# Performance work log

Hardware: AMD Instinct MI355X
Metric: run time of the kernel (lower is better)

The kernel has to match this reference:

```python
import jax, jax.numpy as jnp
import numpy as np

N_NODES = 100000
N_EDGES = 1600000
NFEAT, NHID, NCLASS = 512, 256, 40
ALPHA = 1.0
N_POWERS = 10


def setup_inputs() -> dict:
    key = jax.random.key(0)
    ks = jax.random.split(key, 8)
    x = jax.random.normal(ks[0], (N_NODES, NFEAT), dtype=jnp.float32)
    edge_index = jax.random.randint(ks[1], (2, N_EDGES), 0, N_NODES)
    # Kaiming-ish init, scale = 1/sqrt(fan_in)
    W1 = jax.random.normal(ks[2], (NHID, NFEAT), dtype=jnp.float32) / np.sqrt(NFEAT)
    b1 = jnp.zeros((NHID,), jnp.float32)
    W2 = jax.random.normal(ks[3], (NHID, NHID), dtype=jnp.float32) / np.sqrt(NHID)
    b2 = jnp.zeros((NHID,), jnp.float32)
    W3 = jax.random.normal(ks[4], (NCLASS, NHID), dtype=jnp.float32) / np.sqrt(NHID)
    b3 = jnp.zeros((NCLASS,), jnp.float32)
    return {"x": x, "edge_index": edge_index, "W1": W1, "b1": b1,
            "W2": W2, "b2": b2, "W3": W3, "b3": b3}


def reference(x, edge_index, W1, b1, W2, b2, W3, b3):
    N = x.shape[0]
    # --- build DA-normalized adjacency with self-loops (to_normalized_sparsetensor, mode='DA') ---
    self_loop = jnp.arange(N)
    rows = jnp.concatenate([edge_index[0], self_loop])  # [E+N]
    cols = jnp.concatenate([edge_index[1], self_loop])  # [E+N]
    deg = jax.ops.segment_sum(jnp.ones(rows.shape[0], x.dtype), rows, num_segments=N)
    # DA mode: rows scaled by deg_inv_sqrt^2 == deg^{-1}
    deg_inv = jnp.where(deg > 0, 1.0 / deg, 0.0)
    w = deg_inv[rows]  # per-edge weight, [E+N]

    def spmm(v):  # A @ v, v: [N, C]
        return jax.ops.segment_sum(w[:, None] * v[cols], rows, num_segments=N)

    # --- MLP (dropout=0, eval mode) ---
    h = jax.nn.relu(x @ W1.T + b1)
    h = jax.nn.relu(h @ W2.T + b2)
    h = h @ W3.T + b3  # [N, NCLASS]

    # --- approximate_invphi_x power iteration (beta=0 branch) ---
    c1 = ALPHA / (1.0 + ALPHA)
    c2 = 1.0 / (1.0 + ALPHA)
    invphi = h
    for _ in range(N_POWERS):
        invphi = c1 * spmm(invphi) + c2 * h
    return invphi
```

## Files before the change

### kernel.cpp

```cpp
#include <hip/hip_runtime.h>
#include <type_traits>

#define N_NODES 100000
#define N_EDGES 1600000
#define NFEAT 512
#define NHID 256
#define NCLASS 40
#define NPAD 100096
#define NPAD2 100352

#define NBUCK 196
#define BROWS 512
#define NBLK_BIN 256
#define EPB 6250

#define CDUM 1916000
#define COLN 1916032

#define ZA (N_NODES * 32)
#define ZB (N_NODES * 8)
#define BLK_A 3125
#define BLK_B 391

typedef __bf16 bf16;
typedef __bf16 bf16x8 __attribute__((ext_vector_type(8)));
typedef __bf16 bf16x4 __attribute__((ext_vector_type(4)));
typedef float f32x4 __attribute__((ext_vector_type(4)));
typedef int i32x4 __attribute__((ext_vector_type(4)));


__global__ __launch_bounds__(256) void bin_count(const int* __restrict__ rows,
                                                 int* __restrict__ bcnt) {
    __shared__ int hist[NBUCK];
    int t = threadIdx.x, b = blockIdx.x;
    for (int i = t; i < NBUCK; i += 256) hist[i] = 0;
    __syncthreads();
    int base = b * EPB;
    for (int i = t; i < EPB; i += 256) atomicAdd(&hist[rows[base + i] >> 9], 1);
    __syncthreads();
    for (int i = t; i < NBUCK; i += 256) bcnt[i * NBLK_BIN + b] = hist[i];
}

__global__ __launch_bounds__(256) void bin_scan(const int* __restrict__ bcnt,
                                                int* __restrict__ boff2,
                                                int* __restrict__ btot) {
    __shared__ int sh[256];
    int t = threadIdx.x, bu = blockIdx.x;
    int v = bcnt[bu * 256 + t];
    sh[t] = v;
    __syncthreads();
    for (int off = 1; off < 256; off <<= 1) {
        int x = (t >= off) ? sh[t - off] : 0;
        __syncthreads();
        sh[t] += x;
        __syncthreads();
    }
    boff2[t * NBUCK + bu] = sh[t] - v;
    if (t == 255) btot[bu] = sh[255];
}

__global__ __launch_bounds__(256) void base_scan(const int* __restrict__ btot,
                                                 int* __restrict__ bbase) {
    __shared__ int sh[256];
    int t = threadIdx.x;
    int v = (t < NBUCK) ? btot[t] : 0;
    sh[t] = v;
    __syncthreads();
    for (int off = 1; off < 256; off <<= 1) {
        int x = (t >= off) ? sh[t - off] : 0;
        __syncthreads();
        sh[t] += x;
        __syncthreads();
    }
    if (t < NBUCK) bbase[t] = sh[t] - v;
    if (t == NBUCK - 1) bbase[NBUCK] = sh[t];
}

__global__ __launch_bounds__(256) void bin_scatter(const int* __restrict__ rows,
                                                   const int* __restrict__ cols,
                                                   const int* __restrict__ boff2,
                                                   const int* __restrict__ bbase,
                                                   int* __restrict__ binned) {
    __shared__ int cur[NBUCK];
    int t = threadIdx.x, b = blockIdx.x;
    for (int i = t; i < NBUCK; i += 256) cur[i] = bbase[i] + boff2[b * NBUCK + i];
    __syncthreads();
    int base = b * EPB;
    for (int i = t; i < EPB; i += 256) {
        int r = rows[base + i], c = cols[base + i];
        int pos = atomicAdd(&cur[r >> 9], 1);
        binned[pos] = ((r & 511) << 17) | c;
    }
}

__global__ __launch_bounds__(256) void bucket_csr(const int* __restrict__ binned,
                                                  const int* __restrict__ bbase,
                                                  int2* __restrict__ rowptr2,
                                                  int* __restrict__ colidx,
                                                  float* __restrict__ dinv) {
    __shared__ int cnt[BROWS];
    __shared__ int pref[BROWS];
    __shared__ int psum[256];
    int t = threadIdx.x, bu = blockIdx.x;
    cnt[t] = 0;
    cnt[t + 256] = 0;
    __syncthreads();
    int base = bbase[bu], end = bbase[bu + 1];
    for (int i = base + t; i < end; i += 256) atomicAdd(&cnt[binned[i] >> 17], 1);
    __syncthreads();
    int c0 = cnt[2 * t], c1 = cnt[2 * t + 1];
    int p0 = (c0 + 3) & ~3, p1 = (c1 + 3) & ~3;
    psum[t] = p0 + p1;
    __syncthreads();
    for (int off = 1; off < 256; off <<= 1) {
        int x = (t >= off) ? psum[t - off] : 0;
        __syncthreads();
        psum[t] += x;
        __syncthreads();
    }
    int pex = psum[t] - (p0 + p1);
    pref[2 * t] = pex;
    pref[2 * t + 1] = pex + p0;
    __syncthreads();
    int pbase = (base & ~3) + bu * 1600;
#pragma unroll
    for (int j = 0; j < 2; j++) {
        int idx = t + j * 256;
        int grow = bu * BROWS + idx;
        int rc = cnt[idx];
        int st = pbase + pref[idx];
        int en = st + ((rc + 3) & ~3);
        if (grow < N_NODES) {
            rowptr2[grow] = make_int2(st, en);
            dinv[grow] = 0.5f / (float)(rc + 1);
            for (int k = st + rc; k < en; k++) colidx[k] = N_NODES;
        } else {
            rowptr2[grow] = make_int2(0, 0);
        }
        pref[idx] = st;
    }
    __syncthreads();
    for (int i = base + t; i < end; i += 256) {
        int v = binned[i];
        int pos = atomicAdd(&pref[v >> 17], 1);
        colidx[pos] = v & 0x1FFFF;
    }
}


__global__ void cvt_f2b(const float* __restrict__ a, bf16* __restrict__ b, int n) {
    int i = blockIdx.x * 256 + threadIdx.x;
    if (i < n) b[i] = (bf16)a[i];
}

__global__ void pad_w3(const float* __restrict__ W3, const float* __restrict__ b3,
                       bf16* __restrict__ W3p, float* __restrict__ b3p) {
    int i = blockIdx.x * 256 + threadIdx.x;
    int r = i >> 8;
    W3p[i] = (bf16)((r < NCLASS) ? W3[(size_t)r * 256 + (i & 255)] : 0.f);
    if (i < 64) b3p[i] = (i < NCLASS) ? b3[i] : 0.f;
}

__global__ void zero_dummy(bf16* vAi, bf16* vA0, bf16* vA1,
                           bf16* vBi, bf16* vB0, bf16* vB1,
                           int* colidx) {
    int i = threadIdx.x;
    if (i < 32) {
        vAi[(size_t)ZA + i] = (bf16)0.f;
        vA0[(size_t)ZA + i] = (bf16)0.f;
        vA1[(size_t)ZA + i] = (bf16)0.f;
    }
    if (i < 8) {
        vBi[(size_t)ZB + i] = (bf16)0.f;
        vB0[(size_t)ZB + i] = (bf16)0.f;
        vB1[(size_t)ZB + i] = (bf16)0.f;
        colidx[CDUM + i] = N_NODES;
    }
}


template <int BN, typename AT, bool RELU, int OUTMODE>
__global__ __launch_bounds__(256) void gemm_mfma(const AT* __restrict__ A,
                                                 const bf16* __restrict__ B,
                                                 const float* __restrict__ bias,
                                                 bf16* __restrict__ Cb,
                                                 float* __restrict__ hA,
                                                 float* __restrict__ hB,
                                                 bf16* __restrict__ vA0,
                                                 bf16* __restrict__ vB0,
                                                 int M, int K, int Nout) {
    constexpr int LDT = 40;
    constexpr int WTM = (BN == 128) ? 64 : 32;
    constexpr int MI = WTM / 16;
    constexpr int WMC = 128 / WTM;
    constexpr int BG = BN / 64;
    constexpr bool AF32 = std::is_same<AT, float>::value;
    __shared__ bf16 As[2][128 * LDT];
    __shared__ bf16 Bs[2][BN * LDT];

    int tid = threadIdx.x;
    int wave = tid >> 6, lane = tid & 63;
    int waveM = wave % WMC, waveN = wave / WMC;
    int lc = lane & 15, lq = lane >> 4;

    f32x4 acc[MI][4];
#pragma unroll
    for (int i = 0; i < MI; i++)
#pragma unroll
        for (int j = 0; j < 4; j++) acc[i][j] = (f32x4){0.f, 0.f, 0.f, 0.f};

    int sr = tid >> 2;
    int sc = (tid & 3) * 8;

    float4 pa[2][2];
    bf16x8 ba[2];
    bf16x8 bb[BG];

    auto LOAD = [&](int k0) {
#pragma unroll
        for (int g = 0; g < 2; g++) {
            int grow = blockIdx.y * 128 + sr + g * 64;
            if constexpr (AF32) {
                if (grow < M) {
                    const float* ap = A + (size_t)grow * K + k0 + sc;
                    pa[g][0] = *(const float4*)ap;
                    pa[g][1] = *(const float4*)(ap + 4);
                } else {
                    pa[g][0] = (float4){0.f, 0.f, 0.f, 0.f};
                    pa[g][1] = (float4){0.f, 0.f, 0.f, 0.f};
                }
            } else {
                ba[g] = (grow < M) ? *(const bf16x8*)(A + (size_t)grow * K + k0 + sc)
                                   : (bf16x8){};
            }
        }
#pragma unroll
        for (int g = 0; g < BG; g++) {
            int brow = blockIdx.x * BN + sr + g * 64;
            bb[g] = *(const bf16x8*)(B + (size_t)brow * K + k0 + sc);
        }
    };
    auto STORE = [&](int buf) {
#pragma unroll
        for (int g = 0; g < 2; g++) {
            bf16x8 val;
            if constexpr (AF32) {
                val[0] = (bf16)pa[g][0].x; val[1] = (bf16)pa[g][0].y;
                val[2] = (bf16)pa[g][0].z; val[3] = (bf16)pa[g][0].w;
                val[4] = (bf16)pa[g][1].x; val[5] = (bf16)pa[g][1].y;
                val[6] = (bf16)pa[g][1].z; val[7] = (bf16)pa[g][1].w;
            } else {
                val = ba[g];
            }
            *(bf16x8*)&As[buf][(sr + g * 64) * LDT + sc] = val;
        }
#pragma unroll
        for (int g = 0; g < BG; g++)
            *(bf16x8*)&Bs[buf][(sr + g * 64) * LDT + sc] = bb[g];
    };

    int nt = K / 32;
    LOAD(0);
    STORE(0);
    __syncthreads();
    int cur = 0;
    for (int t = 0; t < nt; t++) {
        if (t + 1 < nt) LOAD((t + 1) * 32);
        bf16x8 af[MI], bfr[4];
#pragma unroll
        for (int i = 0; i < MI; i++)
            af[i] = *(const bf16x8*)&As[cur][(waveM * WTM + i * 16 + lc) * LDT + lq * 8];
#pragma unroll
        for (int j = 0; j < 4; j++)
            bfr[j] = *(const bf16x8*)&Bs[cur][(waveN * 64 + j * 16 + lc) * LDT + lq * 8];
#pragma unroll
        for (int i = 0; i < MI; i++)
#pragma unroll
            for (int j = 0; j < 4; j++)
                acc[i][j] = __builtin_amdgcn_mfma_f32_16x16x32_bf16(af[i], bfr[j], acc[i][j], 0, 0, 0);
        if (t + 1 < nt) STORE(cur ^ 1);
        __syncthreads();
        cur ^= 1;
    }

#pragma unroll
    for (int i = 0; i < MI; i++) {
        int row0 = blockIdx.y * 128 + waveM * WTM + i * 16 + lq * 4;
#pragma unroll
        for (int j = 0; j < 4; j++) {
            int colL = waveN * 64 + j * 16 + lc;
            int col = blockIdx.x * BN + colL;
            float bv = bias[col];
#pragma unroll
            for (int reg = 0; reg < 4; reg++) {
                int rr = row0 + reg;
                if (rr < M) {
                    float v = acc[i][j][reg] + bv;
                    if (RELU) v = v > 0.f ? v : 0.f;
                    if (OUTMODE == 0) {
                        Cb[(size_t)rr * Nout + col] = (bf16)v;
                    } else {
                        if (col < 32) {
                            hA[(size_t)rr * 32 + col] = 0.5f * v;
                            vA0[(size_t)rr * 32 + col] = (bf16)v;
                        } else if (col < NCLASS) {
                            hB[(size_t)rr * 8 + (col - 32)] = 0.5f * v;
                            vB0[(size_t)rr * 8 + (col - 32)] = (bf16)v;
                        }
                    }
                }
            }
        }
    }
}


__global__ __launch_bounds__(256) void spmm_split(const bf16* __restrict__ vA,
                                                  const bf16* __restrict__ vB,
                                                  const float* __restrict__ hA,
                                                  const float* __restrict__ hB,
                                                  const int2* __restrict__ rowptr2,
                                                  const int* __restrict__ colidx,
                                                  const float* __restrict__ dinv,
                                                  bf16* __restrict__ oA,
                                                  bf16* __restrict__ oB,
                                                  float* __restrict__ outF,
                                                  int final_it) {
    int b = blockIdx.x;
    int lane = threadIdx.x & 63;
    const int* cdum = colidx + CDUM;
    if (b < BLK_A) {
        int w = b * 4 + (threadIdx.x >> 6);
        int sub = lane & 7;
        int r = w * 8 + (lane >> 3);
        int2 se = rowptr2[r];
        int sx = se.x, d = se.y - se.x;
        int m = d;
        int x = __shfl_xor(m, 8);  m = m > x ? m : x;
        x = __shfl_xor(m, 16);     m = m > x ? m : x;
        x = __shfl_xor(m, 32);     m = m > x ? m : x;
        float4 hv = *(const float4*)(hA + (size_t)r * 32 + sub * 4);
        float dv = dinv[r];
        bf16x4 sv = *(const bf16x4*)(vA + (size_t)r * 32 + sub * 4);
        float a0 = (float)sv[0], a1 = (float)sv[1], a2 = (float)sv[2], a3 = (float)sv[3];
        i32x4 cc = *(const i32x4*)(d > 0 ? colidx + sx : cdum);
        for (int i = 0; i < m; i += 4) {
            const int* np = (i + 4 < d) ? (colidx + sx + i + 4) : cdum;
            i32x4 cn = *(const i32x4*)np;
            bf16x4 g0 = *(const bf16x4*)(vA + (size_t)cc[0] * 32 + sub * 4);
            bf16x4 g1 = *(const bf16x4*)(vA + (size_t)cc[1] * 32 + sub * 4);
            bf16x4 g2 = *(const bf16x4*)(vA + (size_t)cc[2] * 32 + sub * 4);
            bf16x4 g3 = *(const bf16x4*)(vA + (size_t)cc[3] * 32 + sub * 4);
            a0 += ((float)g0[0] + (float)g1[0]) + ((float)g2[0] + (float)g3[0]);
            a1 += ((float)g0[1] + (float)g1[1]) + ((float)g2[1] + (float)g3[1]);
            a2 += ((float)g0[2] + (float)g1[2]) + ((float)g2[2] + (float)g3[2]);
            a3 += ((float)g0[3] + (float)g1[3]) + ((float)g2[3] + (float)g3[3]);
            cc = cn;
        }
        float r0 = dv * a0 + hv.x;
        float r1 = dv * a1 + hv.y;
        float r2 = dv * a2 + hv.z;
        float r3 = dv * a3 + hv.w;
        if (final_it) {
            *(float4*)(outF + (size_t)r * NCLASS + sub * 4) = (float4){r0, r1, r2, r3};
        } else {
            bf16x4 o;
            o[0] = (bf16)r0; o[1] = (bf16)r1; o[2] = (bf16)r2; o[3] = (bf16)r3;
            *(bf16x4*)(oA + (size_t)r * 32 + sub * 4) = o;
        }
    } else {
        int w = (b - BLK_A) * 4 + (threadIdx.x >> 6);
        int r = w * 64 + lane;
        int rh = (r < N_NODES) ? r : N_NODES;
        int rz = (r < N_NODES) ? r : 0;
        int2 se = rowptr2[r];
        int sx = se.x, d = se.y - se.x;
        int m = d;
#pragma unroll
        for (int off = 1; off < 64; off <<= 1) {
            int x = __shfl_xor(m, off);
            m = m > x ? m : x;
        }
        float4 h0 = *(const float4*)(hB + (size_t)rz * 8);
        float4 h1 = *(const float4*)(hB + (size_t)rz * 8 + 4);
        float dv = dinv[rz];
        bf16x8 sv = *(const bf16x8*)(vB + (size_t)rh * 8);
        float a[8];
#pragma unroll
        for (int k = 0; k < 8; k++) a[k] = (float)sv[k];
        i32x4 cc = *(const i32x4*)(d > 0 ? colidx + sx : cdum);
        for (int i = 0; i < m; i += 4) {
            const int* np = (i + 4 < d) ? (colidx + sx + i + 4) : cdum;
            i32x4 cn = *(const i32x4*)np;
            bf16x8 g0 = *(const bf16x8*)(vB + (size_t)cc[0] * 8);
            bf16x8 g1 = *(const bf16x8*)(vB + (size_t)cc[1] * 8);
            bf16x8 g2 = *(const bf16x8*)(vB + (size_t)cc[2] * 8);
            bf16x8 g3 = *(const bf16x8*)(vB + (size_t)cc[3] * 8);
#pragma unroll
            for (int k = 0; k < 8; k++)
                a[k] += ((float)g0[k] + (float)g1[k]) + ((float)g2[k] + (float)g3[k]);
            cc = cn;
        }
        if (r < N_NODES) {
            float res[8];
            res[0] = dv * a[0] + h0.x; res[1] = dv * a[1] + h0.y;
            res[2] = dv * a[2] + h0.z; res[3] = dv * a[3] + h0.w;
            res[4] = dv * a[4] + h1.x; res[5] = dv * a[5] + h1.y;
            res[6] = dv * a[6] + h1.z; res[7] = dv * a[7] + h1.w;
            if (final_it) {
                *(float4*)(outF + (size_t)r * NCLASS + 32) = (float4){res[0], res[1], res[2], res[3]};
                *(float4*)(outF + (size_t)r * NCLASS + 36) = (float4){res[4], res[5], res[6], res[7]};
            } else {
                bf16x8 o;
#pragma unroll
                for (int k = 0; k < 8; k++) o[k] = (bf16)res[k];
                *(bf16x8*)(oB + (size_t)r * 8) = o;
            }
        }
    }
}


extern "C" void kernel_launch(void* const* d_in, const int* in_sizes, int n_in,
                              void* d_out, int out_size, void* d_ws, size_t ws_size,
                              hipStream_t stream) {
    const float* x  = (const float*)d_in[0];
    const int*   ei = (const int*)d_in[1];
    const float* W1 = (const float*)d_in[2];
    const float* b1 = (const float*)d_in[3];
    const float* W2 = (const float*)d_in[4];
    const float* b2 = (const float*)d_in[5];
    const float* W3 = (const float*)d_in[6];
    const float* b3 = (const float*)d_in[7];
    float* out = (float*)d_out;
    const int* rows = ei;
    const int* cols = ei + N_EDGES;

    char* p = (char*)d_ws;
    bf16* hid1 = (bf16*)p;                 p += (size_t)N_NODES * NHID * 2;
    bf16* hid2 = (bf16*)p;                 p += (size_t)N_NODES * NHID * 2;
    float* hA  = (float*)p;                p += (size_t)N_NODES * 32 * 4;
    float* hB  = (float*)p;                p += (size_t)N_NODES * 8 * 4;
    bf16* vAi  = (bf16*)p;                 p += (size_t)(N_NODES + 1) * 32 * 2;
    bf16* vA0  = (bf16*)p;                 p += (size_t)(N_NODES + 1) * 32 * 2;
    bf16* vA1  = (bf16*)p;                 p += (size_t)(N_NODES + 1) * 32 * 2;
    bf16* vBi  = (bf16*)p;                 p += (size_t)(N_NODES + 1) * 8 * 2;
    bf16* vB0  = (bf16*)p;                 p += (size_t)(N_NODES + 1) * 8 * 2;
    bf16* vB1  = (bf16*)p;                 p += (size_t)(N_NODES + 1) * 8 * 2;
    bf16* W1b  = (bf16*)p;                 p += (size_t)NHID * NFEAT * 2;
    bf16* W2b  = (bf16*)p;                 p += (size_t)NHID * NHID * 2;
    bf16* W3p  = (bf16*)p;                 p += (size_t)64 * NHID * 2;
    float* b3p = (float*)p;                p += 64 * 4;
    int* bcnt    = (int*)p;                p += (size_t)NPAD * 4;
    int2* rowptr2 = (int2*)p;              p += (size_t)NPAD2 * 8;
    int* boff2   = (int*)p;                p += (size_t)N_NODES * 4;
    int* colidx  = (int*)p;                p += (size_t)COLN * 4;
    int* bsum    = (int*)p;                p += 512 * 4;
    float* dinv  = (float*)p;              p += (size_t)N_NODES * 4;

    int* btot  = bsum;
    int* bbase = bsum + 256;
    int* binned = (int*)hid1;

    bin_count<<<NBLK_BIN, 256, 0, stream>>>(rows, bcnt);
    bin_scan<<<NBUCK, 256, 0, stream>>>(bcnt, boff2, btot);
    base_scan<<<1, 256, 0, stream>>>(btot, bbase);
    bin_scatter<<<NBLK_BIN, 256, 0, stream>>>(rows, cols, boff2, bbase, binned);
    bucket_csr<<<NBUCK, 256, 0, stream>>>(binned, bbase, rowptr2, colidx, dinv);

    cvt_f2b<<<(NHID * NFEAT + 255) / 256, 256, 0, stream>>>(W1, W1b, NHID * NFEAT);
    cvt_f2b<<<(NHID * NHID + 255) / 256, 256, 0, stream>>>(W2, W2b, NHID * NHID);
    pad_w3<<<(64 * NHID) / 256, 256, 0, stream>>>(W3, b3, W3p, b3p);

    {
        int M = N_NODES;
        int gy = (M + 127) / 128;
        gemm_mfma<128, float, true, 0><<<dim3(2, gy), 256, 0, stream>>>(
            x, W1b, b1, hid1, nullptr, nullptr, nullptr, nullptr, M, NFEAT, NHID);
        gemm_mfma<128, bf16, true, 0><<<dim3(2, gy), 256, 0, stream>>>(
            hid1, W2b, b2, hid2, nullptr, nullptr, nullptr, nullptr, M, NHID, NHID);
        gemm_mfma<64, bf16, false, 1><<<dim3(1, gy), 256, 0, stream>>>(
            hid2, W3p, b3p, nullptr, hA, hB, vAi, vBi, M, NHID, 64);
    }

    zero_dummy<<<1, 64, 0, stream>>>(vAi, vA0, vA1, vBi, vB0, vB1, colidx);

    const bf16* sA = vAi;
    const bf16* sB = vBi;
    for (int it = 0; it < 10; it++) {
        int fin = (it == 9);
        bf16* dA = (it & 1) ? vA1 : vA0;
        bf16* dB = (it & 1) ? vB1 : vB0;
        spmm_split<<<BLK_A + BLK_B, 256, 0, stream>>>(
            sA, sB, hA, hB, rowptr2, colidx, dinv, dA, dB, out, fin);
        sA = dA;
        sB = dB;
    }
}
```

Baseline: 849.9 us.

## Deepen GEMM prefetch and widen SpMM gathers with two-stage pipelining

The GEMM main loop is unrolled by two and uses ping-pong register sets, so global loads are issued two K-tiles ahead of the MFMA work. The SpMM part A now uses 4 lanes per row with 16-byte bf16x8 gathers instead of 8 lanes with 8-byte gathers, which halves the block count. Both SpMM paths are software-pipelined to keep two groups of 4 neighbor gathers in flight. The costs are higher register pressure, extra padded iterations that read dummy indices, and an early return for out-of-range rows in part A.

```diff
diff --git a/kernel.cpp b/kernel.cpp
--- a/kernel.cpp
+++ b/kernel.cpp
@@ -19,7 +19,7 @@
 
 #define ZA (N_NODES * 32)
 #define ZB (N_NODES * 8)
-#define BLK_A 3125
+#define BLK_A 1563
 #define BLK_B 391
 
 typedef __bf16 bf16;
@@ -212,11 +212,11 @@
     int sr = tid >> 2;
     int sc = (tid & 3) * 8;
 
-    float4 pa[2][2];
-    bf16x8 ba[2];
-    bf16x8 bb[BG];
-
-    auto LOAD = [&](int k0) {
+    float4 paE[2][2], paO[2][2];
+    bf16x8 baE[2], baO[2];
+    bf16x8 bbE[BG], bbO[BG];
+
+    auto LOAD = [&](int k0, float4 (&pa)[2][2], bf16x8 (&ba)[2], bf16x8 (&bb)[BG]) {
 #pragma unroll
         for (int g = 0; g < 2; g++) {
             int grow = blockIdx.y * 128 + sr + g * 64;
@@ -240,7 +240,7 @@
             bb[g] = *(const bf16x8*)(B + (size_t)brow * K + k0 + sc);
         }
     };
-    auto STORE = [&](int buf) {
+    auto STORE = [&](int buf, float4 (&pa)[2][2], bf16x8 (&ba)[2], bf16x8 (&bb)[BG]) {
 #pragma unroll
         for (int g = 0; g < 2; g++) {
             bf16x8 val;
@@ -258,29 +258,36 @@
         for (int g = 0; g < BG; g++)
             *(bf16x8*)&Bs[buf][(sr + g * 64) * LDT + sc] = bb[g];
     };
-
-    int nt = K / 32;
-    LOAD(0);
-    STORE(0);
-    __syncthreads();
-    int cur = 0;
-    for (int t = 0; t < nt; t++) {
-        if (t + 1 < nt) LOAD((t + 1) * 32);
+    auto COMPUTE = [&](int cb) {
         bf16x8 af[MI], bfr[4];
 #pragma unroll
         for (int i = 0; i < MI; i++)
-            af[i] = *(const bf16x8*)&As[cur][(waveM * WTM + i * 16 + lc) * LDT + lq * 8];
+            af[i] = *(const bf16x8*)&As[cb][(waveM * WTM + i * 16 + lc) * LDT + lq * 8];
 #pragma unroll
         for (int j = 0; j < 4; j++)
-            bfr[j] = *(const bf16x8*)&Bs[cur][(waveN * 64 + j * 16 + lc) * LDT + lq * 8];
+            bfr[j] = *(const bf16x8*)&Bs[cb][(waveN * 64 + j * 16 + lc) * LDT + lq * 8];
 #pragma unroll
         for (int i = 0; i < MI; i++)
 #pragma unroll
             for (int j = 0; j < 4; j++)
                 acc[i][j] = __builtin_amdgcn_mfma_f32_16x16x32_bf16(af[i], bfr[j], acc[i][j], 0, 0, 0);
-        if (t + 1 < nt) STORE(cur ^ 1);
-        __syncthreads();
-        cur ^= 1;
+    };
+
+    int nt = K / 32;
+    LOAD(0, paE, baE, bbE);
+    STORE(0, paE, baE, bbE);
+    LOAD(32, paE, baE, bbE);
+    LOAD(64, paO, baO, bbO);
+    __syncthreads();
+    for (int t = 0; t < nt; t += 2) {
+        STORE(1, paE, baE, bbE);
+        if (t + 3 < nt) LOAD((t + 3) * 32, paE, baE, bbE);
+        COMPUTE(0);
+        __syncthreads();
+        if (t + 2 < nt) STORE(0, paO, baO, bbO);
+        if (t + 4 < nt) LOAD((t + 4) * 32, paO, baO, bbO);
+        COMPUTE(1);
+        __syncthreads();
     }
 
 #pragma unroll
@@ -331,47 +338,66 @@
     const int* cdum = colidx + CDUM;
     if (b < BLK_A) {
         int w = b * 4 + (threadIdx.x >> 6);
-        int sub = lane & 7;
-        int r = w * 8 + (lane >> 3);
+        int sub = lane & 3;
+        int r = w * 16 + (lane >> 2);
+        if (r >= N_NODES) return;
         int2 se = rowptr2[r];
         int sx = se.x, d = se.y - se.x;
         int m = d;
-        int x = __shfl_xor(m, 8);  m = m > x ? m : x;
-        x = __shfl_xor(m, 16);     m = m > x ? m : x;
-        x = __shfl_xor(m, 32);     m = m > x ? m : x;
-        float4 hv = *(const float4*)(hA + (size_t)r * 32 + sub * 4);
+#pragma unroll
+        for (int off = 4; off < 64; off <<= 1) {
+            int x = __shfl_xor(m, off);
+            m = m > x ? m : x;
+        }
+        float4 hv0 = *(const float4*)(hA + (size_t)r * 32 + sub * 8);
+        float4 hv1 = *(const float4*)(hA + (size_t)r * 32 + sub * 8 + 4);
         float dv = dinv[r];
-        bf16x4 sv = *(const bf16x4*)(vA + (size_t)r * 32 + sub * 4);
-        float a0 = (float)sv[0], a1 = (float)sv[1], a2 = (float)sv[2], a3 = (float)sv[3];
+        bf16x8 sv = *(const bf16x8*)(vA + (size_t)r * 32 + sub * 8);
+        float a[8];
+#pragma unroll
+        for (int k = 0; k < 8; k++) a[k] = (float)sv[k];
         i32x4 cc = *(const i32x4*)(d > 0 ? colidx + sx : cdum);
-        for (int i = 0; i < m; i += 4) {
-            const int* np = (i + 4 < d) ? (colidx + sx + i + 4) : cdum;
-            i32x4 cn = *(const i32x4*)np;
-            bf16x4 g0 = *(const bf16x4*)(vA + (size_t)cc[0] * 32 + sub * 4);
-            bf16x4 g1 = *(const bf16x4*)(vA + (size_t)cc[1] * 32 + sub * 4);
-            bf16x4 g2 = *(const bf16x4*)(vA + (size_t)cc[2] * 32 + sub * 4);
-            bf16x4 g3 = *(const bf16x4*)(vA + (size_t)cc[3] * 32 + sub * 4);
-            a0 += ((float)g0[0] + (float)g1[0]) + ((float)g2[0] + (float)g3[0]);
-            a1 += ((float)g0[1] + (float)g1[1]) + ((float)g2[1] + (float)g3[1]);
-            a2 += ((float)g0[2] + (float)g1[2]) + ((float)g2[2] + (float)g3[2]);
-            a3 += ((float)g0[3] + (float)g1[3]) + ((float)g2[3] + (float)g3[3]);
-            cc = cn;
-        }
-        float r0 = dv * a0 + hv.x;
-        float r1 = dv * a1 + hv.y;
-        float r2 = dv * a2 + hv.z;
-        float r3 = dv * a3 + hv.w;
+        i32x4 cn = *(const i32x4*)(4 < d ? colidx + sx + 4 : cdum);
+        bf16x8 G0 = *(const bf16x8*)(vA + (size_t)cc[0] * 32 + sub * 8);
+        bf16x8 G1 = *(const bf16x8*)(vA + (size_t)cc[1] * 32 + sub * 8);
+        bf16x8 G2 = *(const bf16x8*)(vA + (size_t)cc[2] * 32 + sub * 8);
+        bf16x8 G3 = *(const bf16x8*)(vA + (size_t)cc[3] * 32 + sub * 8);
+        int m8 = (m + 7) & ~7;
+        for (int i = 0; i < m8; i += 8) {
+            i32x4 ci8 = *(const i32x4*)((i + 8 < d) ? colidx + sx + i + 8 : cdum);
+            bf16x8 H0 = *(const bf16x8*)(vA + (size_t)cn[0] * 32 + sub * 8);
+            bf16x8 H1 = *(const bf16x8*)(vA + (size_t)cn[1] * 32 + sub * 8);
+            bf16x8 H2 = *(const bf16x8*)(vA + (size_t)cn[2] * 32 + sub * 8);
+            bf16x8 H3 = *(const bf16x8*)(vA + (size_t)cn[3] * 32 + sub * 8);
+#pragma unroll
+            for (int k = 0; k < 8; k++)
+                a[k] += ((float)G0[k] + (float)G1[k]) + ((float)G2[k] + (float)G3[k]);
+            cn = *(const i32x4*)((i + 12 < d) ? colidx + sx + i + 12 : cdum);
+            G0 = *(const bf16x8*)(vA + (size_t)ci8[0] * 32 + sub * 8);
+            G1 = *(const bf16x8*)(vA + (size_t)ci8[1] * 32 + sub * 8);
+            G2 = *(const bf16x8*)(vA + (size_t)ci8[2] * 32 + sub * 8);
+            G3 = *(const bf16x8*)(vA + (size_t)ci8[3] * 32 + sub * 8);
+#pragma unroll
+            for (int k = 0; k < 8; k++)
+                a[k] += ((float)H0[k] + (float)H1[k]) + ((float)H2[k] + (float)H3[k]);
+        }
+        float res[8];
+        res[0] = dv * a[0] + hv0.x; res[1] = dv * a[1] + hv0.y;
+        res[2] = dv * a[2] + hv0.z; res[3] = dv * a[3] + hv0.w;
+        res[4] = dv * a[4] + hv1.x; res[5] = dv * a[5] + hv1.y;
+        res[6] = dv * a[6] + hv1.z; res[7] = dv * a[7] + hv1.w;
         if (final_it) {
-            *(float4*)(outF + (size_t)r * NCLASS + sub * 4) = (float4){r0, r1, r2, r3};
+            *(float4*)(outF + (size_t)r * NCLASS + sub * 8) = (float4){res[0], res[1], res[2], res[3]};
+            *(float4*)(outF + (size_t)r * NCLASS + sub * 8 + 4) = (float4){res[4], res[5], res[6], res[7]};
         } else {
-            bf16x4 o;
-            o[0] = (bf16)r0; o[1] = (bf16)r1; o[2] = (bf16)r2; o[3] = (bf16)r3;
-            *(bf16x4*)(oA + (size_t)r * 32 + sub * 4) = o;
+            bf16x8 o;
+#pragma unroll
+            for (int k = 0; k < 8; k++) o[k] = (bf16)res[k];
+            *(bf16x8*)(oA + (size_t)r * 32 + sub * 8) = o;
         }
     } else {
         int w = (b - BLK_A) * 4 + (threadIdx.x >> 6);
         int r = w * 64 + lane;
-        int rh = (r < N_NODES) ? r : N_NODES;
         int rz = (r < N_NODES) ? r : 0;
         int2 se = rowptr2[r];
         int sx = se.x, d = se.y - se.x;
@@ -384,22 +410,34 @@
         float4 h0 = *(const float4*)(hB + (size_t)rz * 8);
         float4 h1 = *(const float4*)(hB + (size_t)rz * 8 + 4);
         float dv = dinv[rz];
-        bf16x8 sv = *(const bf16x8*)(vB + (size_t)rh * 8);
+        bf16x8 sv = *(const bf16x8*)(vB + (size_t)rz * 8);
         float a[8];
 #pragma unroll
         for (int k = 0; k < 8; k++) a[k] = (float)sv[k];
         i32x4 cc = *(const i32x4*)(d > 0 ? colidx + sx : cdum);
-        for (int i = 0; i < m; i += 4) {
-            const int* np = (i + 4 < d) ? (colidx + sx + i + 4) : cdum;
-            i32x4 cn = *(const i32x4*)np;
-            bf16x8 g0 = *(const bf16x8*)(vB + (size_t)cc[0] * 8);
-            bf16x8 g1 = *(const bf16x8*)(vB + (size_t)cc[1] * 8);
-            bf16x8 g2 = *(const bf16x8*)(vB + (size_t)cc[2] * 8);
-            bf16x8 g3 = *(const bf16x8*)(vB + (size_t)cc[3] * 8);
+        i32x4 cn = *(const i32x4*)(4 < d ? colidx + sx + 4 : cdum);
+        bf16x8 G0 = *(const bf16x8*)(vB + (size_t)cc[0] * 8);
+        bf16x8 G1 = *(const bf16x8*)(vB + (size_t)cc[1] * 8);
+        bf16x8 G2 = *(const bf16x8*)(vB + (size_t)cc[2] * 8);
+        bf16x8 G3 = *(const bf16x8*)(vB + (size_t)cc[3] * 8);
+        int m8 = (m + 7) & ~7;
+        for (int i = 0; i < m8; i += 8) {
+            i32x4 ci8 = *(const i32x4*)((i + 8 < d) ? colidx + sx + i + 8 : cdum);
+            bf16x8 H0 = *(const bf16x8*)(vB + (size_t)cn[0] * 8);
+            bf16x8 H1 = *(const bf16x8*)(vB + (size_t)cn[1] * 8);
+            bf16x8 H2 = *(const bf16x8*)(vB + (size_t)cn[2] * 8);
+            bf16x8 H3 = *(const bf16x8*)(vB + (size_t)cn[3] * 8);
 #pragma unroll
             for (int k = 0; k < 8; k++)
-                a[k] += ((float)g0[k] + (float)g1[k]) + ((float)g2[k] + (float)g3[k]);
-            cc = cn;
+                a[k] += ((float)G0[k] + (float)G1[k]) + ((float)G2[k] + (float)G3[k]);
+            cn = *(const i32x4*)((i + 12 < d) ? colidx + sx + i + 12 : cdum);
+            G0 = *(const bf16x8*)(vB + (size_t)ci8[0] * 8);
+            G1 = *(const bf16x8*)(vB + (size_t)ci8[1] * 8);
+            G2 = *(const bf16x8*)(vB + (size_t)ci8[2] * 8);
+            G3 = *(const bf16x8*)(vB + (size_t)ci8[3] * 8);
+#pragma unroll
+            for (int k = 0; k < 8; k++)
+                a[k] += ((float)H0[k] + (float)H1[k]) + ((float)H2[k] + (float)H3[k]);
         }
         if (r < N_NODES) {
             float res[8];
```

Result: faster. 805.0 us (-5.3%).
